# Kernel tuning notes

Hardware: AMD Instinct MI355X
Metric: run time of the kernel (lower is better)

## Reference

```python
import jax, jax.numpy as jnp
import numpy as np

EPS = 1e-8
N_NODES = 100000
N_EDGES = 3200000
S_IN, V_IN = 128, 16
S_OUT, V_OUT = 128, 16
HID = 16          # bottleneck=1 -> max(V_IN, V_OUT)
FRAME_C = 3       # scalarization_vectorization_output_dim
MERGED = HID + S_IN + FRAME_C * 3  # 153


def safe_norm(x, axis):
    return jnp.sqrt(jnp.sum(x * x, axis=axis) + EPS)


def setup_inputs() -> dict:
    key = jax.random.key(0)
    ks = jax.random.split(key, 12)
    scalar_rep = jax.random.normal(ks[0], (N_NODES, S_IN), dtype=jnp.float32)
    vector_rep = jax.random.normal(ks[1], (N_NODES, V_IN, 3), dtype=jnp.float32)
    frames = jax.random.normal(ks[2], (N_EDGES, 3, 3), dtype=jnp.float32)
    edge_index = jax.random.randint(ks[3], (2, N_EDGES), 0, N_NODES, dtype=jnp.int64)
    s = 0.05
    W_down = jax.random.normal(ks[4], (HID, V_IN), dtype=jnp.float32) * s
    W_frames = jax.random.normal(ks[5], (FRAME_C, V_IN), dtype=jnp.float32) * s
    W_scalar = jax.random.normal(ks[6], (S_OUT, MERGED), dtype=jnp.float32) * s
    b_scalar = jnp.zeros((S_OUT,), dtype=jnp.float32)
    W_up = jax.random.normal(ks[7], (V_OUT, HID), dtype=jnp.float32) * s
    W_gate = jax.random.normal(ks[8], (V_OUT, S_OUT), dtype=jnp.float32) * s
    b_gate = jnp.zeros((V_OUT,), dtype=jnp.float32)
    return {"scalar_rep": scalar_rep, "vector_rep": vector_rep, "frames": frames,
            "W_down": W_down, "W_frames": W_frames, "W_scalar": W_scalar,
            "b_scalar": b_scalar, "W_up": W_up, "W_gate": W_gate, "b_gate": b_gate,
            "edge_index": edge_index}


def reference(scalar_rep, vector_rep, frames, W_down, W_frames, W_scalar,
              b_scalar, W_up, W_gate, b_gate, edge_index):
    N = scalar_rep.shape[0]
    row = edge_index[0]
    # vector branch: [N, V, 3] -> [N, 3, V]
    v_pre = jnp.swapaxes(vector_rep, -1, -2)
    vh = jnp.einsum('ntv,hv->nth', v_pre, W_down)          # [N, 3, H]
    vnorm = safe_norm(vh, axis=-2)                          # [N, H]
    vdf = jnp.einsum('ntv,fv->ntf', v_pre, W_frames)        # [N, 3, F=3]
    # scalarize: gather per-edge, frame matmul over spatial dim, scatter-mean
    m = jnp.einsum('est,etf->esf', frames, vdf[row])        # [E, 3(s), 3(f)]
    local = jnp.swapaxes(m, -1, -2).reshape(m.shape[0], 9)  # [E, 9] (f, s) order
    sums = jax.ops.segment_sum(local, row, num_segments=N)
    cnt = jax.ops.segment_sum(jnp.ones((local.shape[0],), dtype=local.dtype),
                              row, num_segments=N)
    scalar_hidden = sums / jnp.maximum(cnt, 1.0)[:, None]   # [N, 9]
    merged = jnp.concatenate([scalar_rep, vnorm, scalar_hidden], axis=-1)  # [N, 153]
    s_out = merged @ W_scalar.T + b_scalar                  # [N, S_OUT]
    # vectorize with sigmoid gate
    v_up = jnp.einsum('nth,vh->ntv', vh, W_up)              # [N, 3, V_OUT]
    v_rep = jnp.swapaxes(v_up, -1, -2)                       # [N, V_OUT, 3]
    gate = jax.nn.silu(s_out) @ W_gate.T + b_gate            # [N, V_OUT]
    v_final = v_rep * jax.nn.sigmoid(gate)[..., None]
    s_final = jax.nn.silu(s_out)
    return s_final, v_final
```

## Files before the change

kernel.cpp:

```cpp
#include <hip/hip_runtime.h>
#include <hip/hip_bf16.h>
#include <math.h>

#define N_NODES 100000
#define N_EDGES 3200000
#define NB 16
#define EPSV 1e-8f

#define NBUCK 782
#define NCHUNK 1280
#define CHUNK_E 2500

#define CE 256
#define RS 264

typedef __attribute__((ext_vector_type(8))) short short8;
typedef __attribute__((ext_vector_type(4))) float f32x4;

static __device__ __forceinline__ unsigned short f2bf(float x) {
  union { float f; unsigned int u; } c; c.f = x;
  unsigned int r = c.u + 0x7fff + ((c.u >> 16) & 1);
  return (unsigned short)(r >> 16);
}

__global__ __launch_bounds__(256) void hist_kernel(const int* __restrict__ row,
                                                   unsigned short* __restrict__ hist) {
  __shared__ int lh[NBUCK];
  for (int i = threadIdx.x; i < NBUCK; i += 256) lh[i] = 0;
  __syncthreads();
  const int c = blockIdx.x;
  const int e1 = c * CHUNK_E + CHUNK_E;
  for (int e = c * CHUNK_E + threadIdx.x; e < e1; e += 256)
    atomicAdd(&lh[row[e] >> 7], 1);
  __syncthreads();
  for (int i = threadIdx.x; i < NBUCK; i += 256)
    hist[(size_t)c * NBUCK + i] = (unsigned short)lh[i];
}

__global__ __launch_bounds__(256) void scanc_kernel(const unsigned short* __restrict__ hist,
                                                    unsigned short* __restrict__ cscan,
                                                    int* __restrict__ total) {
  __shared__ int s[2][NCHUNK];
  const int b = blockIdx.x;
  const int t = threadIdx.x;
  for (int i = t; i < NCHUNK; i += 256) s[0][i] = hist[(size_t)i * NBUCK + b];
  __syncthreads();
  int src = 0;
  for (int off = 1; off < NCHUNK; off <<= 1) {
    int dst = src ^ 1;
    for (int i = t; i < NCHUNK; i += 256)
      s[dst][i] = s[src][i] + ((i >= off) ? s[src][i - off] : 0);
    __syncthreads();
    src = dst;
  }
  for (int i = t; i < NCHUNK; i += 256)
    cscan[(size_t)i * NBUCK + b] = (unsigned short)((i == 0) ? 0 : s[src][i - 1]);
  if (t == 0) total[b] = s[src][NCHUNK - 1];
}

__global__ __launch_bounds__(256) void scanb_kernel(const int* __restrict__ total,
                                                    int* __restrict__ base) {
  __shared__ int s[2][1024];
  const int t = threadIdx.x;
  for (int i = t; i < 1024; i += 256) s[0][i] = (i < NBUCK) ? total[i] : 0;
  __syncthreads();
  int src = 0;
  for (int off = 1; off < 1024; off <<= 1) {
    int dst = src ^ 1;
    for (int i = t; i < 1024; i += 256)
      s[dst][i] = s[src][i] + ((i >= off) ? s[src][i - off] : 0);
    __syncthreads();
    src = dst;
  }
  for (int i = t; i <= NBUCK; i += 256) base[i] = (i == 0) ? 0 : s[src][i - 1];
}

__global__ __launch_bounds__(256) void scatter_kernel(const int* __restrict__ row,
                                                      const unsigned short* __restrict__ hist,
                                                      const unsigned short* __restrict__ cscan,
                                                      const int* __restrict__ base,
                                                      const float* __restrict__ frames,
                                                      unsigned int* __restrict__ payload) {
  __shared__ unsigned int sbuf[CHUNK_E * 5];
  __shared__ int lstart[NBUCK], loff[NBUCK], runG[NBUCK];
  const int c = blockIdx.x, tid = threadIdx.x;

  int (*sc)[1024] = (int(*)[1024])sbuf;
  for (int i = tid; i < 1024; i += 256)
    sc[0][i] = (i < NBUCK) ? (int)hist[(size_t)c * NBUCK + i] : 0;
  __syncthreads();
  int src = 0;
  for (int off = 1; off < 1024; off <<= 1) {
    int dst = src ^ 1;
    for (int i = tid; i < 1024; i += 256)
      sc[dst][i] = sc[src][i] + ((i >= off) ? sc[src][i - off] : 0);
    __syncthreads();
    src = dst;
  }
  for (int i = tid; i < NBUCK; i += 256) {
    int st = (i == 0) ? 0 : sc[src][i - 1];
    lstart[i] = st;
    loff[i] = st;
    runG[i] = base[i] + (int)cscan[(size_t)c * NBUCK + i];
  }
  __syncthreads();

  const int e0 = c * CHUNK_E;
  for (int e = e0 + tid; e < e0 + CHUNK_E; e += 256) {
    int r = row[e];
    const float* f = frames + (size_t)e * 9;
    unsigned int w0 = f2bf(f[0]) | ((unsigned)f2bf(f[1]) << 16);
    unsigned int w1 = f2bf(f[2]) | ((unsigned)f2bf(f[3]) << 16);
    unsigned int w2 = f2bf(f[4]) | ((unsigned)f2bf(f[5]) << 16);
    unsigned int w3 = f2bf(f[6]) | ((unsigned)f2bf(f[7]) << 16);
    unsigned int w4 = f2bf(f[8]) | ((unsigned)(r & 127) << 16);
    int p = atomicAdd(&loff[r >> 7], 1);
    unsigned int* d = sbuf + p * 5;
    d[0] = w0; d[1] = w1; d[2] = w2; d[3] = w3; d[4] = w4;
  }
  __syncthreads();

  const int grp = tid >> 4, gl = tid & 15;
  for (int b = grp; b < NBUCK; b += 16) {
    int ls = lstart[b] * 5;
    int n5 = (loff[b] - lstart[b]) * 5;
    size_t gs = (size_t)runG[b] * 5;
    for (int d = gl; d < n5; d += 16)
      payload[gs + d] = sbuf[ls + d];
  }
}

__global__ __launch_bounds__(256) void reduce_kernel(const unsigned int* __restrict__ payload,
                                                     const int* __restrict__ base,
                                                     float* __restrict__ acc) {
  __shared__ unsigned short stg[2][16][RS];
  const int tid = threadIdx.x;
  const int b = blockIdx.x;
  const int wid = tid >> 6, lane = tid & 63;
  const int lr = lane & 15, lk = lane >> 4;

  for (int i = tid; i < RS; i += 256) {
    stg[0][9][i] = 0x3F80; stg[1][9][i] = 0x3F80;
  }

  const int p0 = base[b], p1 = base[b + 1];
  const int nch = (p1 - p0 + CE - 1) / CE;
  const int s0 = wid * 2;
  const unsigned na = (unsigned)((s0 << 4) | lr);
  const unsigned nbod = (unsigned)(((s0 + 1) << 4) | lr);

  f32x4 c0 = {0.f, 0.f, 0.f, 0.f};
  f32x4 c1 = {0.f, 0.f, 0.f, 0.f};

  auto STAGE = [&](int c, int buf) {
    int p = p0 + c * CE + tid;
    if (p < p1) {
      const unsigned int* s = payload + (size_t)p * 5;
      unsigned int w0 = s[0], w1 = s[1], w2 = s[2], w3 = s[3], w4 = s[4];
      stg[buf][0][tid] = (unsigned short)w0;
      stg[buf][1][tid] = (unsigned short)(w0 >> 16);
      stg[buf][2][tid] = (unsigned short)w1;
      stg[buf][3][tid] = (unsigned short)(w1 >> 16);
      stg[buf][4][tid] = (unsigned short)w2;
      stg[buf][5][tid] = (unsigned short)(w2 >> 16);
      stg[buf][6][tid] = (unsigned short)w3;
      stg[buf][7][tid] = (unsigned short)(w3 >> 16);
      stg[buf][8][tid] = (unsigned short)w4;
      stg[buf][10][tid] = (unsigned short)(w4 >> 16);
    } else {
#pragma unroll
      for (int k = 0; k < 9; ++k) stg[buf][k][tid] = 0;
      stg[buf][10][tid] = 0xFFFF;
    }
  };

  auto COMP = [&](int buf) {
#pragma unroll
    for (int g = 0; g < 8; ++g) {
      short8 bf = *(const short8*)&stg[buf][lr][g * 32 + lk * 8];
      short8 nv = *(const short8*)&stg[buf][10][g * 32 + lk * 8];
      short8 a0, a1;
#pragma unroll
      for (int j = 0; j < 8; ++j) {
        unsigned nid = (unsigned short)nv[j];
        a0[j] = (short)((nid == na)   ? 0x3F80 : 0);
        a1[j] = (short)((nid == nbod) ? 0x3F80 : 0);
      }
      c0 = __builtin_amdgcn_mfma_f32_16x16x32_bf16(a0, bf, c0, 0, 0, 0);
      c1 = __builtin_amdgcn_mfma_f32_16x16x32_bf16(a1, bf, c1, 0, 0, 0);
    }
  };

  if (nch > 0) {
    STAGE(0, 0);
    __syncthreads();
    for (int c = 0; c < nch; ++c) {
      if (c + 1 < nch) STAGE(c + 1, (c + 1) & 1);
      COMP(c & 1);
      __syncthreads();
    }
  }
  const int n0 = b << 7;
  if (lr < 10) {
#pragma unroll
    for (int j = 0; j < 4; ++j) {
      int r = lk * 4 + j;
      int x0 = n0 + s0 * 16 + r;
      int x1 = n0 + (s0 + 1) * 16 + r;
      if (x0 < N_NODES) acc[(size_t)x0 * 10 + lr] = c0[j];
      if (x1 < N_NODES) acc[(size_t)x1 * 10 + lr] = c1[j];
    }
  }
}

__global__ __launch_bounds__(256) void prep_kernel(const float* __restrict__ Ws,
                                                   const float* __restrict__ Wg,
                                                   unsigned short* __restrict__ wsWs,
                                                   unsigned short* __restrict__ wsWg) {
  int idx = blockIdx.x * 256 + threadIdx.x;
  if (idx < 8 * 5 * 512) {
    int j = idx & 7, l = (idx >> 3) & 63, t = idx >> 9;
    int nt = t / 5, kk = t - nt * 5;
    int o = nt * 16 + (l & 15);
    int m = kk * 32 + ((l >> 4) << 3) + j;
    wsWs[idx] = (m < 153) ? f2bf(Ws[o * 153 + m]) : (unsigned short)0;
  }
  if (idx < 4 * 512) {
    int j = idx & 7, l = (idx >> 3) & 63, kk = idx >> 9;
    int v = l & 15;
    int m = kk * 32 + ((l >> 4) << 3) + j;
    wsWg[idx] = f2bf(Wg[v * 128 + m]);
  }
}

__global__ __launch_bounds__(256, 4) void node_kernel(
    const float* __restrict__ scalar_rep,
    const float* __restrict__ vrep,
    const float* __restrict__ Wd,
    const float* __restrict__ Wf,
    const float* __restrict__ bs,
    const float* __restrict__ Wu,
    const float* __restrict__ bg,
    const unsigned short* __restrict__ wsWs,
    const unsigned short* __restrict__ wsWg,
    const float* __restrict__ acc,
    float* __restrict__ out_s,
    float* __restrict__ out_v) {
  __shared__ alignas(16) unsigned short s_mergedb[16 * 168];
  __shared__ alignas(16) unsigned short s_sfb[16 * 136];
  __shared__ float s_vrep[16][48];
  __shared__ float s_vh[16][48];
  __shared__ float s_vdf[16][12];
  __shared__ float s_gate[16][16];
  __shared__ float s_WdT[256], s_WuT[256], s_Wf[48], s_bs[128], s_bg[16];

  const int tid = threadIdx.x;
  {
    int a = tid >> 4, b = tid & 15;
    s_WdT[b * 16 + a] = Wd[tid];
    s_WuT[b * 16 + a] = Wu[tid];
  }
  if (tid < 48) s_Wf[tid] = Wf[tid];
  if (tid < 128) s_bs[tid] = bs[tid];
  if (tid < 16) s_bg[tid] = bg[tid];
  if (tid < 240) {
    int r = tid / 15, c = 153 + tid % 15;
    s_mergedb[r * 168 + c] = 0;
  }

  const int i4 = tid >> 4, j4 = tid & 15;
  const int wid = tid >> 6, lane = tid & 63;
  const int lr = lane & 15, lk = lane >> 4;

  const float4* scalar4 = (const float4*)scalar_rep;
  const float4* vrep4 = (const float4*)vrep;

  for (int g = blockIdx.x; g < N_NODES / NB; g += gridDim.x) {
    const int n0 = g * NB;
    __syncthreads();
    for (int idx = tid; idx < 512; idx += 256) {
      float4 v = scalar4[(size_t)n0 * 32 + idx];
      int r = idx >> 5, c4 = idx & 31;
      unsigned short* d = s_mergedb + r * 168 + c4 * 4;
      d[0] = f2bf(v.x); d[1] = f2bf(v.y); d[2] = f2bf(v.z); d[3] = f2bf(v.w);
    }
    for (int idx = tid; idx < 192; idx += 256)
      ((float4*)s_vrep)[idx] = vrep4[(size_t)n0 * 12 + idx];
    __syncthreads();
    {
      float a0 = 0.f, a1 = 0.f, a2 = 0.f;
#pragma unroll
      for (int v = 0; v < 16; ++v) {
        float w = s_WdT[v * 16 + j4];
        a0 += s_vrep[i4][v * 3 + 0] * w;
        a1 += s_vrep[i4][v * 3 + 1] * w;
        a2 += s_vrep[i4][v * 3 + 2] * w;
      }
      s_vh[i4][j4]      = a0;
      s_vh[i4][16 + j4] = a1;
      s_vh[i4][32 + j4] = a2;
      s_mergedb[i4 * 168 + 128 + j4] = f2bf(sqrtf(a0 * a0 + a1 * a1 + a2 * a2 + EPSV));
    }
    if (j4 < 9) {
      int t = j4 / 3, f = j4 - t * 3;
      float a = 0.f;
#pragma unroll
      for (int v = 0; v < 16; ++v)
        a += s_vrep[i4][v * 3 + t] * s_Wf[f * 16 + v];
      s_vdf[i4][j4] = a;
    }
    __syncthreads();
    if (j4 < 9) {
      int f = j4 / 3, s = j4 - f * 3;
      const float* a = acc + (size_t)(n0 + i4) * 10;
      float c = fmaxf(a[9], 1.0f);
      float sum = a[s * 3 + 0] * s_vdf[i4][0 + f] +
                  a[s * 3 + 1] * s_vdf[i4][3 + f] +
                  a[s * 3 + 2] * s_vdf[i4][6 + f];
      s_mergedb[i4 * 168 + 144 + j4] = f2bf(sum / c);
    }
    __syncthreads();
    {
      const int nt0 = wid * 2;
      short8 afrag[5];
#pragma unroll
      for (int kk = 0; kk < 5; ++kk)
        afrag[kk] = *(const short8*)(s_mergedb + lr * 168 + kk * 32 + lk * 8);
      float b0v = s_bs[nt0 * 16 + lr], b1v = s_bs[nt0 * 16 + 16 + lr];
      f32x4 acc0 = {b0v, b0v, b0v, b0v};
      f32x4 acc1 = {b1v, b1v, b1v, b1v};
#pragma unroll
      for (int kk = 0; kk < 5; ++kk) {
        short8 bf0 = *(const short8*)(wsWs + (((nt0 * 5 + kk) << 6) + lane) * 8);
        short8 bf1 = *(const short8*)(wsWs + ((((nt0 + 1) * 5 + kk) << 6) + lane) * 8);
        acc0 = __builtin_amdgcn_mfma_f32_16x16x32_bf16(afrag[kk], bf0, acc0, 0, 0, 0);
        acc1 = __builtin_amdgcn_mfma_f32_16x16x32_bf16(afrag[kk], bf1, acc1, 0, 0, 0);
      }
#pragma unroll
      for (int j = 0; j < 4; ++j) {
        int node = lk * 4 + j;
        float x0 = acc0[j];
        float sf0 = x0 / (1.0f + __expf(-x0));
        out_s[(size_t)(n0 + node) * 128 + nt0 * 16 + lr] = sf0;
        s_sfb[node * 136 + nt0 * 16 + lr] = f2bf(sf0);
        float x1 = acc1[j];
        float sf1 = x1 / (1.0f + __expf(-x1));
        out_s[(size_t)(n0 + node) * 128 + nt0 * 16 + 16 + lr] = sf1;
        s_sfb[node * 136 + nt0 * 16 + 16 + lr] = f2bf(sf1);
      }
    }
    __syncthreads();
    if (wid == 0) {
      float gb = s_bg[lr];
      f32x4 gacc = {gb, gb, gb, gb};
#pragma unroll
      for (int kk = 0; kk < 4; ++kk) {
        short8 ga = *(const short8*)(s_sfb + lr * 136 + kk * 32 + lk * 8);
        short8 gw = *(const short8*)(wsWg + (((kk << 6) + lane) * 8));
        gacc = __builtin_amdgcn_mfma_f32_16x16x32_bf16(ga, gw, gacc, 0, 0, 0);
      }
#pragma unroll
      for (int j = 0; j < 4; ++j) {
        int node = lk * 4 + j;
        s_gate[node][lr] = 1.0f / (1.0f + __expf(-gacc[j]));
      }
    }
    __syncthreads();
    {
      float b0 = 0.f, b1 = 0.f, b2 = 0.f;
#pragma unroll
      for (int h = 0; h < 16; ++h) {
        float w = s_WuT[h * 16 + j4];
        b0 += s_vh[i4][h]      * w;
        b1 += s_vh[i4][16 + h] * w;
        b2 += s_vh[i4][32 + h] * w;
      }
      float gt = s_gate[i4][j4];
      size_t basep = (size_t)(n0 + i4) * 48 + (size_t)j4 * 3;
      out_v[basep + 0] = b0 * gt;
      out_v[basep + 1] = b1 * gt;
      out_v[basep + 2] = b2 * gt;
    }
  }
}

extern "C" void kernel_launch(void* const* d_in, const int* in_sizes, int n_in,
                              void* d_out, int out_size, void* d_ws, size_t ws_size,
                              hipStream_t stream) {
  const float* scalar_rep = (const float*)d_in[0];
  const float* vector_rep = (const float*)d_in[1];
  const float* frames     = (const float*)d_in[2];
  const float* W_down     = (const float*)d_in[3];
  const float* W_frames   = (const float*)d_in[4];
  const float* W_scalar   = (const float*)d_in[5];
  const float* b_scalar   = (const float*)d_in[6];
  const float* W_up       = (const float*)d_in[7];
  const float* W_gate     = (const float*)d_in[8];
  const float* b_gate     = (const float*)d_in[9];
  const int*   edge_index = (const int*)d_in[10];

  float* out = (float*)d_out;

  unsigned short* hist  = (unsigned short*)d_ws;
  unsigned short* cscan = hist + 1280 * NBUCK;
  int*   total   = (int*)(cscan + 1280 * NBUCK);
  int*   base    = total + 800;
  unsigned int* payload = (unsigned int*)(base + 800);
  float* acc     = (float*)(payload + 16000000);
  unsigned short* wsWs = (unsigned short*)(acc + 1000000);
  unsigned short* wsWg = wsWs + 20480;

  prep_kernel   <<<80,     256, 0, stream>>>(W_scalar, W_gate, wsWs, wsWg);
  hist_kernel   <<<NCHUNK, 256, 0, stream>>>(edge_index, hist);
  scanc_kernel  <<<NBUCK,  256, 0, stream>>>(hist, cscan, total);
  scanb_kernel  <<<1,      256, 0, stream>>>(total, base);
  scatter_kernel<<<NCHUNK, 256, 0, stream>>>(edge_index, hist, cscan, base,
                                             frames, payload);
  reduce_kernel <<<NBUCK,  256, 0, stream>>>(payload, base, acc);

  node_kernel<<<768, 256, 0, stream>>>(
      scalar_rep, vector_rep, W_down, W_frames, b_scalar,
      W_up, b_gate, wsWs, wsWg, acc,
      out, out + (size_t)N_NODES * 128);
}
```

Measured before the change: 219.3 us.

## Move per-chunk local bucket scan into hist kernel, widen scatter blocks to 512

The per-chunk exclusive scan over bucket counts moves out of the scatter kernel and into the histogram kernel, where it is done with a wave-shuffle scan and stored to a new lscan workspace array. The scatter kernel then reads its bucket offsets directly, dropping ten synchronised LDS scan passes. Scatter also runs with 512 threads per block, giving more threads for the edge loop and the copy-out. The cost is extra global writes and reads for lscan, and the larger block may lower occupancy given the kernel's large LDS buffer.

```diff
diff --git a/kernel.cpp b/kernel.cpp
--- a/kernel.cpp
+++ b/kernel.cpp
@@ -24,8 +24,10 @@
 }
 
 __global__ __launch_bounds__(256) void hist_kernel(const int* __restrict__ row,
-                                                   unsigned short* __restrict__ hist) {
+                                                   unsigned short* __restrict__ hist,
+                                                   unsigned short* __restrict__ lscan) {
   __shared__ int lh[NBUCK];
+  __shared__ int wtot[4];
   for (int i = threadIdx.x; i < NBUCK; i += 256) lh[i] = 0;
   __syncthreads();
   const int c = blockIdx.x;
@@ -33,8 +35,30 @@
   for (int e = c * CHUNK_E + threadIdx.x; e < e1; e += 256)
     atomicAdd(&lh[row[e] >> 7], 1);
   __syncthreads();
-  for (int i = threadIdx.x; i < NBUCK; i += 256)
-    hist[(size_t)c * NBUCK + i] = (unsigned short)lh[i];
+  const int t = threadIdx.x, lane = t & 63, wid = t >> 6;
+  const int b0 = t * 4;
+  int h[4];
+#pragma unroll
+  for (int j = 0; j < 4; ++j) h[j] = (b0 + j < NBUCK) ? lh[b0 + j] : 0;
+  int s = h[0] + h[1] + h[2] + h[3];
+  int incl = s;
+#pragma unroll
+  for (int d = 1; d < 64; d <<= 1) {
+    int o = __shfl_up(incl, d);
+    if (lane >= d) incl += o;
+  }
+  if (lane == 63) wtot[wid] = incl;
+  __syncthreads();
+  int pre = incl - s;
+  for (int w = 0; w < wid; ++w) pre += wtot[w];
+#pragma unroll
+  for (int j = 0; j < 4; ++j) {
+    if (b0 + j < NBUCK) {
+      hist [(size_t)c * NBUCK + b0 + j] = (unsigned short)h[j];
+      lscan[(size_t)c * NBUCK + b0 + j] = (unsigned short)pre;
+    }
+    pre += h[j];
+  }
 }
 
 __global__ __launch_bounds__(256) void scanc_kernel(const unsigned short* __restrict__ hist,
@@ -75,8 +99,8 @@
   for (int i = t; i <= NBUCK; i += 256) base[i] = (i == 0) ? 0 : s[src][i - 1];
 }
 
-__global__ __launch_bounds__(256) void scatter_kernel(const int* __restrict__ row,
-                                                      const unsigned short* __restrict__ hist,
+__global__ __launch_bounds__(512) void scatter_kernel(const int* __restrict__ row,
+                                                      const unsigned short* __restrict__ lscan,
                                                       const unsigned short* __restrict__ cscan,
                                                       const int* __restrict__ base,
                                                       const float* __restrict__ frames,
@@ -85,20 +109,8 @@
   __shared__ int lstart[NBUCK], loff[NBUCK], runG[NBUCK];
   const int c = blockIdx.x, tid = threadIdx.x;
 
-  int (*sc)[1024] = (int(*)[1024])sbuf;
-  for (int i = tid; i < 1024; i += 256)
-    sc[0][i] = (i < NBUCK) ? (int)hist[(size_t)c * NBUCK + i] : 0;
-  __syncthreads();
-  int src = 0;
-  for (int off = 1; off < 1024; off <<= 1) {
-    int dst = src ^ 1;
-    for (int i = tid; i < 1024; i += 256)
-      sc[dst][i] = sc[src][i] + ((i >= off) ? sc[src][i - off] : 0);
-    __syncthreads();
-    src = dst;
-  }
-  for (int i = tid; i < NBUCK; i += 256) {
-    int st = (i == 0) ? 0 : sc[src][i - 1];
+  for (int i = tid; i < NBUCK; i += 512) {
+    int st = (int)lscan[(size_t)c * NBUCK + i];
     lstart[i] = st;
     loff[i] = st;
     runG[i] = base[i] + (int)cscan[(size_t)c * NBUCK + i];
@@ -106,7 +118,7 @@
   __syncthreads();
 
   const int e0 = c * CHUNK_E;
-  for (int e = e0 + tid; e < e0 + CHUNK_E; e += 256) {
+  for (int e = e0 + tid; e < e0 + CHUNK_E; e += 512) {
     int r = row[e];
     const float* f = frames + (size_t)e * 9;
     unsigned int w0 = f2bf(f[0]) | ((unsigned)f2bf(f[1]) << 16);
@@ -121,7 +133,7 @@
   __syncthreads();
 
   const int grp = tid >> 4, gl = tid & 15;
-  for (int b = grp; b < NBUCK; b += 16) {
+  for (int b = grp; b < NBUCK; b += 32) {
     int ls = lstart[b] * 5;
     int n5 = (loff[b] - lstart[b]) * 5;
     size_t gs = (size_t)runG[b] * 5;
@@ -402,8 +414,9 @@
   float* out = (float*)d_out;
 
   unsigned short* hist  = (unsigned short*)d_ws;
-  unsigned short* cscan = hist + 1280 * NBUCK;
-  int*   total   = (int*)(cscan + 1280 * NBUCK);
+  unsigned short* lscan = hist  + (size_t)NCHUNK * NBUCK;
+  unsigned short* cscan = lscan + (size_t)NCHUNK * NBUCK;
+  int*   total   = (int*)(cscan + (size_t)NCHUNK * NBUCK);
   int*   base    = total + 800;
   unsigned int* payload = (unsigned int*)(base + 800);
   float* acc     = (float*)(payload + 16000000);
@@ -411,10 +424,10 @@
   unsigned short* wsWg = wsWs + 20480;
 
   prep_kernel   <<<80,     256, 0, stream>>>(W_scalar, W_gate, wsWs, wsWg);
-  hist_kernel   <<<NCHUNK, 256, 0, stream>>>(edge_index, hist);
+  hist_kernel   <<<NCHUNK, 256, 0, stream>>>(edge_index, hist, lscan);
   scanc_kernel  <<<NBUCK,  256, 0, stream>>>(hist, cscan, total);
   scanb_kernel  <<<1,      256, 0, stream>>>(total, base);
-  scatter_kernel<<<NCHUNK, 256, 0, stream>>>(edge_index, hist, cscan, base,
+  scatter_kernel<<<NCHUNK, 512, 0, stream>>>(edge_index, lscan, cscan, base,
                                              frames, payload);
   reduce_kernel <<<NBUCK,  256, 0, stream>>>(payload, base, acc);
 
```

Measured after the change: 198.7 us. -9.4%, faster.
